# Performance work log

Hardware: AMD Instinct MI355X
Metric: run time of the kernel (lower is better)

The kernel has to match this reference:

```python
import jax, jax.numpy as jnp
import numpy as np

N = 50000   # nodes
E = 800000  # edges
D_IN = 128
DIMS = [(D_IN, 256), (256, 128), (128, 64), (64, 40)]  # per-layer (d_in, d_out)
EPS = 1e-5


def setup_inputs() -> dict:
    key = jax.random.key(0)
    ks = jax.random.split(key, 40)
    inp = {}
    inp["x"] = jax.random.normal(ks[0], (N, D_IN), jnp.float32)
    inp["edge_index"] = jax.random.randint(ks[1], (2, E), 0, N, dtype=jnp.int32)
    ki = 2
    for li, (din, dout) in enumerate(DIMS, 1):
        s = 1.0 / np.sqrt(din)
        inp[f"Wl{li}"] = jax.random.uniform(ks[ki], (din, dout), jnp.float32, -s, s); ki += 1  # SAGE lin_l (neighbor agg), has bias
        inp[f"bl{li}"] = jnp.zeros((dout,), jnp.float32)
        inp[f"Wr{li}"] = jax.random.uniform(ks[ki], (din, dout), jnp.float32, -s, s); ki += 1  # SAGE lin_r (root), no bias
        inp[f"Ws{li}"] = jax.random.uniform(ks[ki], (din, dout), jnp.float32, -s, s); ki += 1  # skip Linear
        inp[f"bs{li}"] = jnp.zeros((dout,), jnp.float32)
        if li < 4:  # BatchNorm only after layers 1-3
            inp[f"g{li}"] = jnp.ones((dout,), jnp.float32)
            inp[f"be{li}"] = jnp.zeros((dout,), jnp.float32)
    return inp


def reference(x, edge_index, Wl1, bl1, Wr1, Ws1, bs1, g1, be1,
              Wl2, bl2, Wr2, Ws2, bs2, g2, be2,
              Wl3, bl3, Wr3, Ws3, bs3, g3, be3,
              Wl4, bl4, Wr4, Ws4, bs4):
    src, dst = edge_index[0], edge_index[1]
    # in-degree counts for mean aggregation (clamped to 1 like PyG)
    cnt = jax.ops.segment_sum(jnp.ones((E,), x.dtype), dst, num_segments=N)
    cnt = jnp.maximum(cnt, 1.0)[:, None]

    def sage(h, Wl, bl, Wr):
        # mean over incoming neighbors, then lin_l(agg) + lin_r(root)
        agg = jax.ops.segment_sum(h[src], dst, num_segments=N) / cnt
        return agg @ Wl + bl + h @ Wr

    def bn(h, g, b):
        mu = h.mean(0)
        var = h.var(0)  # biased variance, as torch BN training mode
        return (h - mu) * jax.lax.rsqrt(var + EPS) * g + b

    h = jax.nn.relu(sage(x, Wl1, bl1, Wr1) + x @ Ws1 + bs1)
    h = bn(h, g1, be1)
    h = jax.nn.relu(sage(h, Wl2, bl2, Wr2) + h @ Ws2 + bs2)
    h = bn(h, g2, be2)
    h = jax.nn.relu(sage(h, Wl3, bl3, Wr3) + h @ Ws3 + bs3)
    h = bn(h, g3, be3)
    return sage(h, Wl4, bl4, Wr4) + h @ Ws4 + bs4
```

## Files before the change

### kernel.cpp

```cpp
#include <hip/hip_runtime.h>


static constexpr int NN = 50000;
static constexpr int NE = 800000;
static constexpr int NP = 50048;

typedef __attribute__((ext_vector_type(8))) short short8;
typedef __attribute__((ext_vector_type(4))) float f32x4;

__device__ __forceinline__ unsigned short bf16rne(float x) {
  unsigned u = __float_as_uint(x);
  return (unsigned short)((u + 0x7FFFu + ((u >> 16) & 1u)) >> 16);
}
__device__ __forceinline__ float bf2f(unsigned short h) {
  return __uint_as_float(((unsigned)h) << 16);
}

__global__ void count_deg(const int* __restrict__ dst, int* __restrict__ cnt, int E) {
  int e = blockIdx.x * blockDim.x + threadIdx.x;
  if (e < E) atomicAdd(&cnt[dst[e]], 1);
}

__global__ __launch_bounds__(1024) void scan_block(const int* __restrict__ cnt,
                                                   int* __restrict__ excl,
                                                   int* __restrict__ btot, int n) {
  __shared__ int lds[1024];
  int i = blockIdx.x * 1024 + threadIdx.x;
  int v = (i < n) ? cnt[i] : 0;
  lds[threadIdx.x] = v;
  __syncthreads();
#pragma unroll
  for (int off = 1; off < 1024; off <<= 1) {
    int t = 0;
    if ((int)threadIdx.x >= off) t = lds[threadIdx.x - off];
    __syncthreads();
    lds[threadIdx.x] += t;
    __syncthreads();
  }
  if (i < n) excl[i] = lds[threadIdx.x] - v;
  if (threadIdx.x == 1023) btot[blockIdx.x] = lds[1023];
}

__global__ void scan_tops(int* __restrict__ btot, int nb) {
  int t = threadIdx.x;
  int v = (t < nb) ? btot[t] : 0;
  int own = v;
#pragma unroll
  for (int off = 1; off < 64; off <<= 1) {
    int u = __shfl_up(v, off);
    if (t >= off) v += u;
  }
  if (t < nb) btot[t] = v - own;
}

__global__ void finalize_csr(int* __restrict__ offs, const int* __restrict__ btot,
                             const int* __restrict__ cnt, int* __restrict__ cursor,
                             float* __restrict__ inv, int n) {
  int i = blockIdx.x * blockDim.x + threadIdx.x;
  if (i < n) {
    int o = offs[i] + btot[i >> 10];
    offs[i] = o;
    cursor[i] = o;
    int c = cnt[i];
    inv[i] = 1.0f / (float)(c > 0 ? c : 1);
  }
}

__global__ void fill_adj(const int* __restrict__ src, const int* __restrict__ dst,
                         int* __restrict__ cursor, int* __restrict__ adj, int E) {
  int e = blockIdx.x * blockDim.x + threadIdx.x;
  if (e < E) {
    int p = atomicAdd(&cursor[dst[e]], 1);
    adj[p] = src[e];
  }
}

__global__ void pack_x(const float* __restrict__ x, ushort* __restrict__ xP,
                       ushort* __restrict__ xb, int N) {
  int gid = blockIdx.x * 256 + threadIdx.x;
  int row = gid >> 4, kb = gid & 15;
  if (row >= NP) return;
  float v[8];
  if (row < N) {
    float4 a = *(const float4*)&x[(size_t)row * 128 + kb * 8];
    float4 b = *(const float4*)&x[(size_t)row * 128 + kb * 8 + 4];
    v[0]=a.x; v[1]=a.y; v[2]=a.z; v[3]=a.w; v[4]=b.x; v[5]=b.y; v[6]=b.z; v[7]=b.w;
  } else {
#pragma unroll
    for (int j = 0; j < 8; ++j) v[j] = 0.f;
  }
  short8 H, L;
#pragma unroll
  for (int j = 0; j < 8; ++j) {
    unsigned short h = bf16rne(v[j]);
    H[j] = (short)h;
    L[j] = (short)bf16rne(v[j] - bf2f(h));
  }
  *(short8*)&xP[((size_t)(kb * 2) * NP + row) * 8] = H;
  *(short8*)&xP[((size_t)(kb * 2 + 1) * NP + row) * 8] = L;
  *(short8*)&xb[(size_t)row * 128 + kb * 8] = H;
}

template <int L1V>
__global__ void prep_w(const float* __restrict__ Wl, const float* __restrict__ Wr,
                       const float* __restrict__ Wsk, const float* __restrict__ ab,
                       ushort* __restrict__ Wp, int K, int K1, int M, int Mp, int Mpad) {
  int gid = blockIdx.x * 256 + threadIdx.x;
  int col = gid % Mpad, kb = gid / Mpad;
  if (kb >= (K >> 3)) return;
  short8 H, L;
#pragma unroll
  for (int j = 0; j < 8; ++j) {
    int k = kb * 8 + j;
    float v = 0.f;
    if (col < Mp) {
      if (L1V) {
        v = (k < K1) ? Wl[(size_t)k * M + col]
                     : Wr[(size_t)(k - K1) * M + col] + Wsk[(size_t)(k - K1) * M + col];
      } else {
        float w = (col < M) ? Wl[(size_t)k * M + col]
                            : Wr[(size_t)k * M + (col - M)] + Wsk[(size_t)k * M + (col - M)];
        v = ab[k] * w;
      }
    }
    unsigned short h = bf16rne(v);
    H[j] = (short)h;
    L[j] = (short)bf16rne(v - bf2f(h));
  }
  *(short8*)&Wp[((size_t)(kb * 2) * Mpad + col) * 8] = H;
  *(short8*)&Wp[((size_t)(kb * 2 + 1) * Mpad + col) * 8] = L;
}

__global__ void prep_bias(const float* __restrict__ Wl, const float* __restrict__ Wr,
                          const float* __restrict__ Wsk, const float* __restrict__ bl,
                          const float* __restrict__ bs, const float* __restrict__ ab,
                          float* __restrict__ bias2, int K, int M) {
  int c = blockIdx.x;
  int k = threadIdx.x;
  float va = 0.f, vd = 0.f;
  if (k < K) {
    float b = ab[K + k];
    vd = b * Wl[(size_t)k * M + c];
    va = b * (Wr[(size_t)k * M + c] + Wsk[(size_t)k * M + c]);
  }
  __shared__ float r[512];
  r[k] = va;
  r[256 + k] = vd;
  __syncthreads();
  for (int off = 128; off > 0; off >>= 1) {
    if (k < off) {
      r[k] += r[k + off];
      r[256 + k] += r[256 + k + off];
    }
    __syncthreads();
  }
  if (k == 0) {
    bias2[c] = bl[c] + bs[c] + r[0];
    bias2[M + c] = r[256];
  }
}

__global__ __launch_bounds__(256) void aggregate1(
    const ushort* __restrict__ xb, const int* __restrict__ adj,
    const int* __restrict__ offs, const int* __restrict__ cnt,
    const float* __restrict__ inv, ushort* __restrict__ aggP,
    float* __restrict__ sums, int N) {
  const int tid = threadIdx.x;
  if (blockIdx.x == 0) {
    for (int j = tid; j < 512; j += 256) sums[j] = 0.f;
  }
  const int n = blockIdx.x * 8 + (tid >> 5);
  const int c4 = (tid & 31) * 4;
  float s0 = 0.f, s1 = 0.f, s2 = 0.f, s3 = 0.f;
  float invn = 0.f;
  if (n < N) {
    invn = inv[n];
    int off = offs[n], deg = cnt[n];
    const ushort* __restrict__ hp = xb + c4;
    int i = 0;
    for (; i + 4 <= deg; i += 4) {
      int a0 = adj[off + i + 0];
      int a1 = adj[off + i + 1];
      int a2 = adj[off + i + 2];
      int a3 = adj[off + i + 3];
      ushort4 v0 = *(const ushort4*)&hp[(size_t)a0 * 128];
      ushort4 v1 = *(const ushort4*)&hp[(size_t)a1 * 128];
      ushort4 v2 = *(const ushort4*)&hp[(size_t)a2 * 128];
      ushort4 v3 = *(const ushort4*)&hp[(size_t)a3 * 128];
      s0 += (bf2f(v0.x) + bf2f(v1.x)) + (bf2f(v2.x) + bf2f(v3.x));
      s1 += (bf2f(v0.y) + bf2f(v1.y)) + (bf2f(v2.y) + bf2f(v3.y));
      s2 += (bf2f(v0.z) + bf2f(v1.z)) + (bf2f(v2.z) + bf2f(v3.z));
      s3 += (bf2f(v0.w) + bf2f(v1.w)) + (bf2f(v2.w) + bf2f(v3.w));
    }
    for (; i < deg; ++i) {
      ushort4 v = *(const ushort4*)&hp[(size_t)adj[off + i] * 128];
      s0 += bf2f(v.x); s1 += bf2f(v.y); s2 += bf2f(v.z); s3 += bf2f(v.w);
    }
  }
  float m0 = s0 * invn, m1 = s1 * invn, m2 = s2 * invn, m3 = s3 * invn;
  ushort4 H, L;
  H.x = bf16rne(m0); L.x = bf16rne(m0 - bf2f(H.x));
  H.y = bf16rne(m1); L.y = bf16rne(m1 - bf2f(H.y));
  H.z = bf16rne(m2); L.z = bf16rne(m2 - bf2f(H.z));
  H.w = bf16rne(m3); L.w = bf16rne(m3 - bf2f(H.w));
  const int kb = c4 >> 3, sl = c4 & 7;
  size_t chunk = ((size_t)(kb * 2) * NP + n) * 8 + sl;
  *(ushort4*)&aggP[chunk] = H;
  *(ushort4*)&aggP[chunk + (size_t)NP * 8] = L;
}

template <int TWO_A, int EPI, int NK32, int KT1>
__global__ __launch_bounds__(256) void gemm_pk(
    const ushort* __restrict__ A1, const ushort* __restrict__ A2,
    const ushort* __restrict__ B, const float* __restrict__ bl,
    const float* __restrict__ bs, ushort* __restrict__ OutL,
    float* __restrict__ OutR, ushort* __restrict__ OutP,
    float* __restrict__ sums, int N, int M, int Mp, int Mpad) {
  const int tid = threadIdx.x;
  const int l = tid & 63;
  const int w = tid >> 6;
  const int wr = w >> 1, wc = w & 1;
  const int l16 = l & 15, lh = l >> 4;
  const int row0 = blockIdx.x * 128, col0 = blockIdx.y * 128;

  const f32x4 z4 = {0.f, 0.f, 0.f, 0.f};
  f32x4 acc[4][4];
#pragma unroll
  for (int m = 0; m < 4; ++m)
#pragma unroll
    for (int n = 0; n < 4; ++n) acc[m][n] = z4;

  const int arow = row0 + wr * 64 + l16;
  const int bcol = col0 + wc * 64 + l16;

#pragma unroll 2
  for (int it = 0; it < NK32; ++it) {
    const int kbase = it * 32;
    const ushort* Ap = A1;
    int kloc = kbase;
    if (TWO_A && kbase >= KT1) { Ap = A2; kloc = kbase - KT1; }
    const int akb = (kloc >> 3) + lh;
    const int bkb = (kbase >> 3) + lh;
    const ushort* a_hi = Ap + ((size_t)(akb * 2) * NP + arow) * 8;
    const ushort* a_lo = a_hi + (size_t)NP * 8;
    const ushort* b_hi = B + ((size_t)(bkb * 2) * Mpad + bcol) * 8;
    const ushort* b_lo = b_hi + (size_t)Mpad * 8;

    short8 ah[4], al[4], bh[4], blo[4];
#pragma unroll
    for (int m = 0; m < 4; ++m) {
      ah[m] = *(const short8*)(a_hi + m * 128);
      al[m] = *(const short8*)(a_lo + m * 128);
    }
#pragma unroll
    for (int n = 0; n < 4; ++n) {
      bh[n] = *(const short8*)(b_hi + n * 128);
      blo[n] = *(const short8*)(b_lo + n * 128);
    }
#pragma unroll
    for (int m = 0; m < 4; ++m)
#pragma unroll
      for (int n = 0; n < 4; ++n) {
        acc[m][n] = __builtin_amdgcn_mfma_f32_16x16x32_bf16(ah[m], bh[n], acc[m][n], 0, 0, 0);
        acc[m][n] = __builtin_amdgcn_mfma_f32_16x16x32_bf16(ah[m], blo[n], acc[m][n], 0, 0, 0);
        acc[m][n] = __builtin_amdgcn_mfma_f32_16x16x32_bf16(al[m], bh[n], acc[m][n], 0, 0, 0);
      }
  }

  const int lr = lh * 4;
  if (EPI) {
    __shared__ float st[2048];
    float cs[4] = {0.f, 0.f, 0.f, 0.f}, cq[4] = {0.f, 0.f, 0.f, 0.f};
#pragma unroll
    for (int n = 0; n < 4; ++n) {
      int col = col0 + wc * 64 + n * 16 + l16;
      bool cok = col < Mp;
      float bias = cok ? (bl[col] + bs[col]) : 0.f;
      int cb = col >> 3, ch = col & 7;
      size_t hbase = ((size_t)(cb * 2) * NP) * 8 + ch;
      size_t lbase = hbase + (size_t)NP * 8;
#pragma unroll
      for (int m = 0; m < 4; ++m)
#pragma unroll
        for (int i = 0; i < 4; ++i) {
          int row = row0 + wr * 64 + m * 16 + lr + i;
          float v = acc[m][n][i] + bias;
          v = fmaxf(v, 0.f);
          if (cok && row < N) {
            unsigned short hh = bf16rne(v);
            OutP[hbase + (size_t)row * 8] = hh;
            OutP[lbase + (size_t)row * 8] = bf16rne(v - bf2f(hh));
            cs[n] += v;
            cq[n] += v * v;
          }
        }
    }
    int slot = wr * 4 + lh;
#pragma unroll
    for (int n = 0; n < 4; ++n) {
      int c = wc * 64 + n * 16 + l16;
      st[c * 8 + slot] = cs[n];
      st[1024 + c * 8 + slot] = cq[n];
    }
    __syncthreads();
    if (tid < 128) {
      float s1 = 0.f, s2 = 0.f;
#pragma unroll
      for (int t2 = 0; t2 < 8; ++t2) {
        s1 += st[tid * 8 + t2];
        s2 += st[1024 + tid * 8 + t2];
      }
      int c = col0 + tid;
      if (c < Mp) {
        atomicAdd(&sums[c], s1);
        atomicAdd(&sums[Mp + c], s2);
      }
    }
  } else {
#pragma unroll
    for (int n = 0; n < 4; ++n) {
      int col = col0 + wc * 64 + n * 16 + l16;
      if (col >= Mp) continue;
      bool isL = col < M;
      int colR = col - M;
#pragma unroll
      for (int m = 0; m < 4; ++m)
#pragma unroll
        for (int i = 0; i < 4; ++i) {
          int row = row0 + wr * 64 + m * 16 + lr + i;
          if (row < N) {
            float v = acc[m][n][i];
            if (isL) OutL[(size_t)row * M + col] = bf16rne(v);
            else     OutR[(size_t)row * M + colR] = v;
          }
        }
    }
  }
}

template <int G, int LOGG, int M, int RELU, int STATS, int PACK>
__global__ __launch_bounds__(256) void combine(
    const ushort* __restrict__ Zl, const float* __restrict__ Zr,
    const int* __restrict__ adj, const int* __restrict__ offs,
    const int* __restrict__ cnt, const float* __restrict__ inv,
    const float* __restrict__ bias2, float* __restrict__ outF,
    ushort* __restrict__ outP, float* __restrict__ sums, int N) {
  constexpr int S = 256 / G;
  const int tid = threadIdx.x;
  const int c4 = (tid & (G - 1)) * 4;
  const int sub = tid >> LOGG;
  const bool act = (c4 < M);
  float ba0 = 0, ba1 = 0, ba2 = 0, ba3 = 0, bd0 = 0, bd1 = 0, bd2 = 0, bd3 = 0;
  if (act) {
    float4 ba = *(const float4*)&bias2[c4];
    float4 bd = *(const float4*)&bias2[M + c4];
    ba0 = ba.x; ba1 = ba.y; ba2 = ba.z; ba3 = ba.w;
    bd0 = bd.x; bd1 = bd.y; bd2 = bd.z; bd3 = bd.w;
  }
  float cs[4] = {0.f, 0.f, 0.f, 0.f}, cq[4] = {0.f, 0.f, 0.f, 0.f};
  const ushort* __restrict__ Zc = Zl + c4;
  for (int n = blockIdx.x * S + sub; n < N; n += gridDim.x * S) {
    if (act) {
      int off = offs[n], deg = cnt[n];
      float s0 = 0.f, s1 = 0.f, s2 = 0.f, s3 = 0.f;
      int i = 0;
      for (; i + 4 <= deg; i += 4) {
        int a0 = adj[off + i + 0];
        int a1 = adj[off + i + 1];
        int a2 = adj[off + i + 2];
        int a3 = adj[off + i + 3];
        ushort4 v0 = *(const ushort4*)&Zc[(size_t)a0 * M];
        ushort4 v1 = *(const ushort4*)&Zc[(size_t)a1 * M];
        ushort4 v2 = *(const ushort4*)&Zc[(size_t)a2 * M];
        ushort4 v3 = *(const ushort4*)&Zc[(size_t)a3 * M];
        s0 += (bf2f(v0.x) + bf2f(v1.x)) + (bf2f(v2.x) + bf2f(v3.x));
        s1 += (bf2f(v0.y) + bf2f(v1.y)) + (bf2f(v2.y) + bf2f(v3.y));
        s2 += (bf2f(v0.z) + bf2f(v1.z)) + (bf2f(v2.z) + bf2f(v3.z));
        s3 += (bf2f(v0.w) + bf2f(v1.w)) + (bf2f(v2.w) + bf2f(v3.w));
      }
      for (; i < deg; ++i) {
        ushort4 v = *(const ushort4*)&Zc[(size_t)adj[off + i] * M];
        s0 += bf2f(v.x); s1 += bf2f(v.y); s2 += bf2f(v.z); s3 += bf2f(v.w);
      }
      float invn = inv[n];
      float4 zr = *(const float4*)&Zr[(size_t)n * M + c4];
      float y0 = fmaf(s0, invn, zr.x + ba0);
      float y1 = fmaf(s1, invn, zr.y + ba1);
      float y2 = fmaf(s2, invn, zr.z + ba2);
      float y3 = fmaf(s3, invn, zr.w + ba3);
      if (deg > 0) { y0 += bd0; y1 += bd1; y2 += bd2; y3 += bd3; }
      if (RELU) {
        y0 = fmaxf(y0, 0.f); y1 = fmaxf(y1, 0.f);
        y2 = fmaxf(y2, 0.f); y3 = fmaxf(y3, 0.f);
      }
      if (PACK) {
        ushort4 H, L;
        H.x = bf16rne(y0); L.x = bf16rne(y0 - bf2f(H.x));
        H.y = bf16rne(y1); L.y = bf16rne(y1 - bf2f(H.y));
        H.z = bf16rne(y2); L.z = bf16rne(y2 - bf2f(H.z));
        H.w = bf16rne(y3); L.w = bf16rne(y3 - bf2f(H.w));
        const int kb = c4 >> 3, sl = c4 & 7;
        size_t chunk = ((size_t)(kb * 2) * NP + n) * 8 + sl;
        *(ushort4*)&outP[chunk] = H;
        *(ushort4*)&outP[chunk + (size_t)NP * 8] = L;
      } else {
        *(float4*)&outF[(size_t)n * M + c4] = make_float4(y0, y1, y2, y3);
      }
      if (STATS) {
        cs[0] += y0; cs[1] += y1; cs[2] += y2; cs[3] += y3;
        cq[0] += y0 * y0; cq[1] += y1 * y1; cq[2] += y2 * y2; cq[3] += y3 * y3;
      }
    }
  }
  if (STATS) {
    __shared__ float st1[S * M], st2[S * M];
#pragma unroll
    for (int j = 0; j < 4; ++j) {
      st1[sub * M + c4 + j] = cs[j];
      st2[sub * M + c4 + j] = cq[j];
    }
    __syncthreads();
    if (tid < M) {
      float s1 = 0.f, s2 = 0.f;
#pragma unroll
      for (int t2 = 0; t2 < S; ++t2) {
        s1 += st1[t2 * M + tid];
        s2 += st2[t2 * M + tid];
      }
      atomicAdd(&sums[tid], s1);
      atomicAdd(&sums[M + tid], s2);
    }
  }
}

__global__ void bn_affine(float* __restrict__ sums, const float* __restrict__ g,
                          const float* __restrict__ be, float* __restrict__ ab,
                          int M, float invN) {
  int j = threadIdx.x;
  if (j < M) {
    float s1 = sums[j], s2 = sums[M + j];
    float mu = s1 * invN;
    float var = fmaf(-mu, mu, s2 * invN);
    float a = g[j] / sqrtf(var + 1e-5f);
    ab[j] = a;
    ab[M + j] = fmaf(-mu, a, be[j]);
    sums[j] = 0.f;
    sums[M + j] = 0.f;
  }
}

extern "C" void kernel_launch(void* const* d_in, const int* in_sizes, int n_in,
                              void* d_out, int out_size, void* d_ws, size_t ws_size,
                              hipStream_t stream) {
  const int N = NN, E = NE;
  const float* x = (const float*)d_in[0];
  const int* ei = (const int*)d_in[1];
  const int* srcs = ei;
  const int* dsts = ei + E;

  const float* Wl1 = (const float*)d_in[2];
  const float* bl1 = (const float*)d_in[3];
  const float* Wr1 = (const float*)d_in[4];
  const float* Ws1 = (const float*)d_in[5];
  const float* bs1 = (const float*)d_in[6];
  const float* g1  = (const float*)d_in[7];
  const float* be1 = (const float*)d_in[8];
  const float* Wl2 = (const float*)d_in[9];
  const float* bl2 = (const float*)d_in[10];
  const float* Wr2 = (const float*)d_in[11];
  const float* Ws2 = (const float*)d_in[12];
  const float* bs2 = (const float*)d_in[13];
  const float* g2  = (const float*)d_in[14];
  const float* be2 = (const float*)d_in[15];
  const float* Wl3 = (const float*)d_in[16];
  const float* bl3 = (const float*)d_in[17];
  const float* Wr3 = (const float*)d_in[18];
  const float* Ws3 = (const float*)d_in[19];
  const float* bs3 = (const float*)d_in[20];
  const float* g3  = (const float*)d_in[21];
  const float* be3 = (const float*)d_in[22];
  const float* Wl4 = (const float*)d_in[23];
  const float* bl4 = (const float*)d_in[24];
  const float* Wr4 = (const float*)d_in[25];
  const float* Ws4 = (const float*)d_in[26];
  const float* bs4 = (const float*)d_in[27];

  char* wsB = (char*)d_ws;
  ushort* hAP = (ushort*)wsB;
  ushort* hCP = hAP;
  ushort* xP  = (ushort*)(wsB + 51249152);
  ushort* hBP = xP;
  char* regC  = wsB + 51249152 + 25624576;
  ushort* aggP = (ushort*)regC;
  float* Zr   = (float*)regC;
  char* regD  = regC + 25624576;
  ushort* xb  = (ushort*)regD;
  ushort* Zl  = (ushort*)regD;
  char* p = regD + (size_t)NP * 128 * 2;
  ushort* W1p = (ushort*)p; p += 262144;
  ushort* W2p = (ushort*)p; p += 262144;
  ushort* W3p = (ushort*)p; p += 65536;
  ushort* W4p = (ushort*)p; p += 32768;
  float* sums = (float*)p; p += 512 * 4;
  float* ab   = (float*)p; p += 512 * 4;
  float* bias2 = (float*)p; p += 256 * 4;
  float* invc = (float*)p; p += (size_t)N * 4;
  int* cnt    = (int*)p; p += (size_t)N * 4;
  int* offs   = (int*)p; p += (size_t)N * 4;
  int* cursor = (int*)p; p += (size_t)N * 4;
  int* btot   = (int*)p; p += 256;
  int* adj    = (int*)p;

  hipMemsetAsync(cnt, 0, sizeof(int) * N, stream);
  int eb = (E + 255) / 256;
  int nb = (N + 1023) / 1024;
  count_deg<<<eb, 256, 0, stream>>>(dsts, cnt, E);
  scan_block<<<nb, 1024, 0, stream>>>(cnt, offs, btot, N);
  scan_tops<<<1, 64, 0, stream>>>(btot, nb);
  finalize_csr<<<(N + 255) / 256, 256, 0, stream>>>(offs, btot, cnt, cursor, invc, N);
  fill_adj<<<eb, 256, 0, stream>>>(srcs, dsts, cursor, adj, E);

  pack_x<<<NP * 16 / 256, 256, 0, stream>>>(x, xP, xb, N);
  prep_w<1><<<32 * 256 / 256, 256, 0, stream>>>(Wl1, Wr1, Ws1, nullptr, W1p,
                                                256, 128, 256, 256, 256);

  const int RB = NP / 128;
  const float invN = 1.0f / (float)N;

  aggregate1<<<NP / 8, 256, 0, stream>>>(xb, adj, offs, cnt, invc, aggP, sums, N);
  gemm_pk<1, 1, 8, 128><<<dim3(RB, 2), 256, 0, stream>>>(
      aggP, xP, W1p, bl1, bs1, nullptr, nullptr, hAP, sums, N, 256, 256, 256);
  bn_affine<<<1, 256, 0, stream>>>(sums, g1, be1, ab, 256, invN);

  prep_w<0><<<32 * 256 / 256, 256, 0, stream>>>(Wl2, Wr2, Ws2, ab, W2p,
                                                256, 0, 128, 256, 256);
  prep_bias<<<128, 256, 0, stream>>>(Wl2, Wr2, Ws2, bl2, bs2, ab, bias2, 256, 128);
  gemm_pk<0, 0, 8, 0><<<dim3(RB, 2), 256, 0, stream>>>(
      hAP, nullptr, W2p, nullptr, nullptr, Zl, Zr, nullptr, nullptr, N, 128, 256, 256);
  combine<32, 5, 128, 1, 1, 1><<<2048, 256, 0, stream>>>(
      Zl, Zr, adj, offs, cnt, invc, bias2, nullptr, hBP, sums, N);
  bn_affine<<<1, 128, 0, stream>>>(sums, g2, be2, ab, 128, invN);

  prep_w<0><<<16 * 128 / 256, 256, 0, stream>>>(Wl3, Wr3, Ws3, ab, W3p,
                                                128, 0, 64, 128, 128);
  prep_bias<<<64, 256, 0, stream>>>(Wl3, Wr3, Ws3, bl3, bs3, ab, bias2, 128, 64);
  gemm_pk<0, 0, 4, 0><<<dim3(RB, 1), 256, 0, stream>>>(
      hBP, nullptr, W3p, nullptr, nullptr, Zl, Zr, nullptr, nullptr, N, 64, 128, 128);
  combine<16, 4, 64, 1, 1, 1><<<2048, 256, 0, stream>>>(
      Zl, Zr, adj, offs, cnt, invc, bias2, nullptr, hCP, sums, N);
  bn_affine<<<1, 64, 0, stream>>>(sums, g3, be3, ab, 64, invN);

  prep_w<0><<<8 * 128 / 256, 256, 0, stream>>>(Wl4, Wr4, Ws4, ab, W4p,
                                               64, 0, 40, 80, 128);
  prep_bias<<<40, 256, 0, stream>>>(Wl4, Wr4, Ws4, bl4, bs4, ab, bias2, 64, 40);
  gemm_pk<0, 0, 2, 0><<<dim3(RB, 1), 256, 0, stream>>>(
      hCP, nullptr, W4p, nullptr, nullptr, Zl, Zr, nullptr, nullptr, N, 40, 80, 128);
  combine<16, 4, 40, 0, 0, 0><<<2048, 256, 0, stream>>>(
      Zl, Zr, adj, offs, cnt, invc, bias2, (float*)d_out, nullptr, nullptr, N);
}
```

Baseline: 570.7 us.

## Partition gather tables into 32-column slabs mapped to XCDs for L2 locality

Stores the bf16 gather sources (xb and Zl) as column slabs of 32 features, each slab a contiguous NP×32 table. Aggregate and combine kernels then assign each XCD (blockIdx & 7) a fixed slab, so each XCD's L2 only caches a fraction of the feature table during random neighbor gathers. This trades more passes over the adjacency lists (each slab re-reads adj/offs) and narrower per-node work for better L2 hit rates. It relies on round-robin block-to-XCD dispatch, which is assumed rather than guaranteed.

```diff
diff --git a/kernel.cpp b/kernel.cpp
--- a/kernel.cpp
+++ b/kernel.cpp
@@ -7,6 +7,8 @@
 
 typedef __attribute__((ext_vector_type(8))) short short8;
 typedef __attribute__((ext_vector_type(4))) float f32x4;
+
+static constexpr size_t PSTRIDE = (size_t)NP * 32;
 
 __device__ __forceinline__ unsigned short bf16rne(float x) {
   unsigned u = __float_as_uint(x);
@@ -98,7 +100,7 @@
   }
   *(short8*)&xP[((size_t)(kb * 2) * NP + row) * 8] = H;
   *(short8*)&xP[((size_t)(kb * 2 + 1) * NP + row) * 8] = L;
-  *(short8*)&xb[(size_t)row * 128 + kb * 8] = H;
+  *(short8*)&xb[(size_t)(kb >> 2) * PSTRIDE + (size_t)row * 32 + (kb & 3) * 8] = H;
 }
 
 template <int L1V>
@@ -160,7 +162,7 @@
   }
 }
 
-__global__ __launch_bounds__(256) void aggregate1(
+__global__ __launch_bounds__(256) void aggregate1p(
     const ushort* __restrict__ xb, const int* __restrict__ adj,
     const int* __restrict__ offs, const int* __restrict__ cnt,
     const float* __restrict__ inv, ushort* __restrict__ aggP,
@@ -169,44 +171,51 @@
   if (blockIdx.x == 0) {
     for (int j = tid; j < 512; j += 256) sums[j] = 0.f;
   }
-  const int n = blockIdx.x * 8 + (tid >> 5);
-  const int c4 = (tid & 31) * 4;
-  float s0 = 0.f, s1 = 0.f, s2 = 0.f, s3 = 0.f;
-  float invn = 0.f;
-  if (n < N) {
-    invn = inv[n];
-    int off = offs[n], deg = cnt[n];
-    const ushort* __restrict__ hp = xb + c4;
-    int i = 0;
-    for (; i + 4 <= deg; i += 4) {
-      int a0 = adj[off + i + 0];
-      int a1 = adj[off + i + 1];
-      int a2 = adj[off + i + 2];
-      int a3 = adj[off + i + 3];
-      ushort4 v0 = *(const ushort4*)&hp[(size_t)a0 * 128];
-      ushort4 v1 = *(const ushort4*)&hp[(size_t)a1 * 128];
-      ushort4 v2 = *(const ushort4*)&hp[(size_t)a2 * 128];
-      ushort4 v3 = *(const ushort4*)&hp[(size_t)a3 * 128];
-      s0 += (bf2f(v0.x) + bf2f(v1.x)) + (bf2f(v2.x) + bf2f(v3.x));
-      s1 += (bf2f(v0.y) + bf2f(v1.y)) + (bf2f(v2.y) + bf2f(v3.y));
-      s2 += (bf2f(v0.z) + bf2f(v1.z)) + (bf2f(v2.z) + bf2f(v3.z));
-      s3 += (bf2f(v0.w) + bf2f(v1.w)) + (bf2f(v2.w) + bf2f(v3.w));
-    }
-    for (; i < deg; ++i) {
-      ushort4 v = *(const ushort4*)&hp[(size_t)adj[off + i] * 128];
-      s0 += bf2f(v.x); s1 += bf2f(v.y); s2 += bf2f(v.z); s3 += bf2f(v.w);
-    }
-  }
-  float m0 = s0 * invn, m1 = s1 * invn, m2 = s2 * invn, m3 = s3 * invn;
-  ushort4 H, L;
-  H.x = bf16rne(m0); L.x = bf16rne(m0 - bf2f(H.x));
-  H.y = bf16rne(m1); L.y = bf16rne(m1 - bf2f(H.y));
-  H.z = bf16rne(m2); L.z = bf16rne(m2 - bf2f(H.z));
-  H.w = bf16rne(m3); L.w = bf16rne(m3 - bf2f(H.w));
-  const int kb = c4 >> 3, sl = c4 & 7;
-  size_t chunk = ((size_t)(kb * 2) * NP + n) * 8 + sl;
-  *(ushort4*)&aggP[chunk] = H;
-  *(ushort4*)&aggP[chunk + (size_t)NP * 8] = L;
+  const int xcd = blockIdx.x & 7;
+  const int p = xcd & 3;
+  const int setIdx = (blockIdx.x >> 3) * 2 + (xcd >> 2);
+  const int nSets = (gridDim.x >> 3) * 2;
+  const int sub = tid >> 3;
+  const int c4 = (tid & 7) * 4;
+  const int col = p * 32 + c4;
+  const ushort* __restrict__ tab = xb + (size_t)p * PSTRIDE + c4;
+  const int kb = col >> 3, sl = col & 7;
+
+  for (int n = setIdx * 32 + sub; n < NP; n += nSets * 32) {
+    float s0 = 0.f, s1 = 0.f, s2 = 0.f, s3 = 0.f, invn = 0.f;
+    if (n < N) {
+      invn = inv[n];
+      int off = offs[n], deg = cnt[n];
+      int i = 0;
+      for (; i + 4 <= deg; i += 4) {
+        int a0 = adj[off + i + 0];
+        int a1 = adj[off + i + 1];
+        int a2 = adj[off + i + 2];
+        int a3 = adj[off + i + 3];
+        ushort4 v0 = *(const ushort4*)&tab[(size_t)a0 * 32];
+        ushort4 v1 = *(const ushort4*)&tab[(size_t)a1 * 32];
+        ushort4 v2 = *(const ushort4*)&tab[(size_t)a2 * 32];
+        ushort4 v3 = *(const ushort4*)&tab[(size_t)a3 * 32];
+        s0 += (bf2f(v0.x) + bf2f(v1.x)) + (bf2f(v2.x) + bf2f(v3.x));
+        s1 += (bf2f(v0.y) + bf2f(v1.y)) + (bf2f(v2.y) + bf2f(v3.y));
+        s2 += (bf2f(v0.z) + bf2f(v1.z)) + (bf2f(v2.z) + bf2f(v3.z));
+        s3 += (bf2f(v0.w) + bf2f(v1.w)) + (bf2f(v2.w) + bf2f(v3.w));
+      }
+      for (; i < deg; ++i) {
+        ushort4 v = *(const ushort4*)&tab[(size_t)adj[off + i] * 32];
+        s0 += bf2f(v.x); s1 += bf2f(v.y); s2 += bf2f(v.z); s3 += bf2f(v.w);
+      }
+    }
+    float m0 = s0 * invn, m1 = s1 * invn, m2 = s2 * invn, m3 = s3 * invn;
+    ushort4 H, L;
+    H.x = bf16rne(m0); L.x = bf16rne(m0 - bf2f(H.x));
+    H.y = bf16rne(m1); L.y = bf16rne(m1 - bf2f(H.y));
+    H.z = bf16rne(m2); L.z = bf16rne(m2 - bf2f(H.z));
+    H.w = bf16rne(m3); L.w = bf16rne(m3 - bf2f(H.w));
+    size_t chunk = ((size_t)(kb * 2) * NP + n) * 8 + sl;
+    *(ushort4*)&aggP[chunk] = H;
+    *(ushort4*)&aggP[chunk + (size_t)NP * 8] = L;
+  }
 }
 
 template <int TWO_A, int EPI, int NK32, int KT1>
@@ -323,6 +332,7 @@
       if (col >= Mp) continue;
       bool isL = col < M;
       int colR = col - M;
+      size_t lblk = (size_t)(col >> 5) * PSTRIDE + (col & 31);
 #pragma unroll
       for (int m = 0; m < 4; ++m)
 #pragma unroll
@@ -330,7 +340,7 @@
           int row = row0 + wr * 64 + m * 16 + lr + i;
           if (row < N) {
             float v = acc[m][n][i];
-            if (isL) OutL[(size_t)row * M + col] = bf16rne(v);
+            if (isL) OutL[lblk + (size_t)row * 32] = bf16rne(v);
             else     OutR[(size_t)row * M + colR] = v;
           }
         }
@@ -338,28 +348,37 @@
   }
 }
 
-template <int G, int LOGG, int M, int RELU, int STATS, int PACK>
-__global__ __launch_bounds__(256) void combine(
+template <int NPLOG, int M, int RELU, int STATS, int PACK>
+__global__ __launch_bounds__(256) void combineP(
     const ushort* __restrict__ Zl, const float* __restrict__ Zr,
     const int* __restrict__ adj, const int* __restrict__ offs,
     const int* __restrict__ cnt, const float* __restrict__ inv,
     const float* __restrict__ bias2, float* __restrict__ outF,
     ushort* __restrict__ outP, float* __restrict__ sums, int N) {
-  constexpr int S = 256 / G;
+  constexpr int NPASS = 1 << NPLOG;
+  constexpr int XCDG = 8 >> NPLOG;
   const int tid = threadIdx.x;
-  const int c4 = (tid & (G - 1)) * 4;
-  const int sub = tid >> LOGG;
-  const bool act = (c4 < M);
+  const int xcd = blockIdx.x & 7;
+  const int p = xcd & (NPASS - 1);
+  const int setIdx = (blockIdx.x >> 3) * XCDG + (xcd >> NPLOG);
+  const int nSets = (gridDim.x >> 3) * XCDG;
+  const int sub = tid >> 3;
+  const int c4 = (tid & 7) * 4;
+  const int col = p * 32 + c4;
+  const bool act = col < M;
+
   float ba0 = 0, ba1 = 0, ba2 = 0, ba3 = 0, bd0 = 0, bd1 = 0, bd2 = 0, bd3 = 0;
   if (act) {
-    float4 ba = *(const float4*)&bias2[c4];
-    float4 bd = *(const float4*)&bias2[M + c4];
+    float4 ba = *(const float4*)&bias2[col];
+    float4 bd = *(const float4*)&bias2[M + col];
     ba0 = ba.x; ba1 = ba.y; ba2 = ba.z; ba3 = ba.w;
     bd0 = bd.x; bd1 = bd.y; bd2 = bd.z; bd3 = bd.w;
   }
   float cs[4] = {0.f, 0.f, 0.f, 0.f}, cq[4] = {0.f, 0.f, 0.f, 0.f};
-  const ushort* __restrict__ Zc = Zl + c4;
-  for (int n = blockIdx.x * S + sub; n < N; n += gridDim.x * S) {
+  const ushort* __restrict__ tab = Zl + (size_t)p * PSTRIDE + c4;
+  const int kb = col >> 3, sl = col & 7;
+
+  for (int n = setIdx * 32 + sub; n < N; n += nSets * 32) {
     if (act) {
       int off = offs[n], deg = cnt[n];
       float s0 = 0.f, s1 = 0.f, s2 = 0.f, s3 = 0.f;
@@ -369,21 +388,21 @@
         int a1 = adj[off + i + 1];
         int a2 = adj[off + i + 2];
         int a3 = adj[off + i + 3];
-        ushort4 v0 = *(const ushort4*)&Zc[(size_t)a0 * M];
-        ushort4 v1 = *(const ushort4*)&Zc[(size_t)a1 * M];
-        ushort4 v2 = *(const ushort4*)&Zc[(size_t)a2 * M];
-        ushort4 v3 = *(const ushort4*)&Zc[(size_t)a3 * M];
+        ushort4 v0 = *(const ushort4*)&tab[(size_t)a0 * 32];
+        ushort4 v1 = *(const ushort4*)&tab[(size_t)a1 * 32];
+        ushort4 v2 = *(const ushort4*)&tab[(size_t)a2 * 32];
+        ushort4 v3 = *(const ushort4*)&tab[(size_t)a3 * 32];
         s0 += (bf2f(v0.x) + bf2f(v1.x)) + (bf2f(v2.x) + bf2f(v3.x));
         s1 += (bf2f(v0.y) + bf2f(v1.y)) + (bf2f(v2.y) + bf2f(v3.y));
         s2 += (bf2f(v0.z) + bf2f(v1.z)) + (bf2f(v2.z) + bf2f(v3.z));
         s3 += (bf2f(v0.w) + bf2f(v1.w)) + (bf2f(v2.w) + bf2f(v3.w));
       }
       for (; i < deg; ++i) {
-        ushort4 v = *(const ushort4*)&Zc[(size_t)adj[off + i] * M];
+        ushort4 v = *(const ushort4*)&tab[(size_t)adj[off + i] * 32];
         s0 += bf2f(v.x); s1 += bf2f(v.y); s2 += bf2f(v.z); s3 += bf2f(v.w);
       }
       float invn = inv[n];
-      float4 zr = *(const float4*)&Zr[(size_t)n * M + c4];
+      float4 zr = *(const float4*)&Zr[(size_t)n * M + col];
       float y0 = fmaf(s0, invn, zr.x + ba0);
       float y1 = fmaf(s1, invn, zr.y + ba1);
       float y2 = fmaf(s2, invn, zr.z + ba2);
@@ -399,12 +418,11 @@
         H.y = bf16rne(y1); L.y = bf16rne(y1 - bf2f(H.y));
         H.z = bf16rne(y2); L.z = bf16rne(y2 - bf2f(H.z));
         H.w = bf16rne(y3); L.w = bf16rne(y3 - bf2f(H.w));
-        const int kb = c4 >> 3, sl = c4 & 7;
         size_t chunk = ((size_t)(kb * 2) * NP + n) * 8 + sl;
         *(ushort4*)&outP[chunk] = H;
         *(ushort4*)&outP[chunk + (size_t)NP * 8] = L;
       } else {
-        *(float4*)&outF[(size_t)n * M + c4] = make_float4(y0, y1, y2, y3);
+        *(float4*)&outF[(size_t)n * M + col] = make_float4(y0, y1, y2, y3);
       }
       if (STATS) {
         cs[0] += y0; cs[1] += y1; cs[2] += y2; cs[3] += y3;
@@ -413,22 +431,25 @@
     }
   }
   if (STATS) {
-    __shared__ float st1[S * M], st2[S * M];
+    __shared__ float st1[32 * 32], st2[32 * 32];
 #pragma unroll
     for (int j = 0; j < 4; ++j) {
-      st1[sub * M + c4 + j] = cs[j];
-      st2[sub * M + c4 + j] = cq[j];
+      st1[sub * 32 + c4 + j] = cs[j];
+      st2[sub * 32 + c4 + j] = cq[j];
     }
     __syncthreads();
-    if (tid < M) {
+    if (tid < 32) {
       float s1 = 0.f, s2 = 0.f;
 #pragma unroll
-      for (int t2 = 0; t2 < S; ++t2) {
-        s1 += st1[t2 * M + tid];
-        s2 += st2[t2 * M + tid];
-      }
-      atomicAdd(&sums[tid], s1);
-      atomicAdd(&sums[M + tid], s2);
+      for (int t2 = 0; t2 < 32; ++t2) {
+        s1 += st1[t2 * 32 + tid];
+        s2 += st2[t2 * 32 + tid];
+      }
+      int c = p * 32 + tid;
+      if (c < M) {
+        atomicAdd(&sums[c], s1);
+        atomicAdd(&sums[M + c], s2);
+      }
     }
   }
 }
@@ -525,9 +546,10 @@
                                                 256, 128, 256, 256, 256);
 
   const int RB = NP / 128;
+  const int GP = 4096;
   const float invN = 1.0f / (float)N;
 
-  aggregate1<<<NP / 8, 256, 0, stream>>>(xb, adj, offs, cnt, invc, aggP, sums, N);
+  aggregate1p<<<GP, 256, 0, stream>>>(xb, adj, offs, cnt, invc, aggP, sums, N);
   gemm_pk<1, 1, 8, 128><<<dim3(RB, 2), 256, 0, stream>>>(
       aggP, xP, W1p, bl1, bs1, nullptr, nullptr, hAP, sums, N, 256, 256, 256);
   bn_affine<<<1, 256, 0, stream>>>(sums, g1, be1, ab, 256, invN);
@@ -537,7 +559,7 @@
   prep_bias<<<128, 256, 0, stream>>>(Wl2, Wr2, Ws2, bl2, bs2, ab, bias2, 256, 128);
   gemm_pk<0, 0, 8, 0><<<dim3(RB, 2), 256, 0, stream>>>(
       hAP, nullptr, W2p, nullptr, nullptr, Zl, Zr, nullptr, nullptr, N, 128, 256, 256);
-  combine<32, 5, 128, 1, 1, 1><<<2048, 256, 0, stream>>>(
+  combineP<2, 128, 1, 1, 1><<<GP, 256, 0, stream>>>(
       Zl, Zr, adj, offs, cnt, invc, bias2, nullptr, hBP, sums, N);
   bn_affine<<<1, 128, 0, stream>>>(sums, g2, be2, ab, 128, invN);
 
@@ -546,7 +568,7 @@
   prep_bias<<<64, 256, 0, stream>>>(Wl3, Wr3, Ws3, bl3, bs3, ab, bias2, 128, 64);
   gemm_pk<0, 0, 4, 0><<<dim3(RB, 1), 256, 0, stream>>>(
       hBP, nullptr, W3p, nullptr, nullptr, Zl, Zr, nullptr, nullptr, N, 64, 128, 128);
-  combine<16, 4, 64, 1, 1, 1><<<2048, 256, 0, stream>>>(
+  combineP<1, 64, 1, 1, 1><<<GP, 256, 0, stream>>>(
       Zl, Zr, adj, offs, cnt, invc, bias2, nullptr, hCP, sums, N);
   bn_affine<<<1, 64, 0, stream>>>(sums, g3, be3, ab, 64, invN);
 
@@ -555,6 +577,6 @@
   prep_bias<<<40, 256, 0, stream>>>(Wl4, Wr4, Ws4, bl4, bs4, ab, bias2, 64, 40);
   gemm_pk<0, 0, 2, 0><<<dim3(RB, 1), 256, 0, stream>>>(
       hCP, nullptr, W4p, nullptr, nullptr, Zl, Zr, nullptr, nullptr, N, 40, 80, 128);
-  combine<16, 4, 40, 0, 0, 0><<<2048, 256, 0, stream>>>(
+  combineP<1, 40, 0, 0, 0><<<GP, 256, 0, stream>>>(
       Zl, Zr, adj, offs, cnt, invc, bias2, (float*)d_out, nullptr, nullptr, N);
 }
```

After: 539.3 us. -5.5%, faster.
